# Optimization experiments

Measured on AMD Instinct MI355X. Metric: run time of the kernel, lower is better.

The kernel has to match this reference:

```python
import jax, jax.numpy as jnp
import numpy as np

CAPACITY = 0.5  # top_k = int(seq_len * capacity)

def setup_inputs() -> dict:
    key = jax.random.key(0)
    k1, k2, k3, k4 = jax.random.split(key, 4)
    b, s, d, d_ff = 4, 4096, 1024, 4096
    x = jax.random.normal(k1, (b, s, d), dtype=jnp.float32)
    mask = jnp.ones((b, s), dtype=jnp.bool_)
    # learned params: router (Linear(d,1,bias=False)) and the block MLP
    Wr = jax.random.normal(k2, (d, 1), dtype=jnp.float32) * (d ** -0.5)
    W1 = jax.random.normal(k3, (d, d_ff), dtype=jnp.float32) * (d ** -0.5)
    W2 = jax.random.normal(k4, (d_ff, d), dtype=jnp.float32) * (d_ff ** -0.5)
    return {"x": x, "mask": mask, "Wr": Wr, "W1": W1, "W2": W2}

def reference(x, mask, Wr, W1, W2):
    b, s, d = x.shape
    top_k = int(s * CAPACITY)
    # router logits [b, s]
    logits = (x @ Wr)[..., 0]
    # top-k over sequence dim (torch sorted=False; softmax/gather are
    # permutation-equivariant so sorted top_k gives identical results)
    vals, idx = jax.lax.top_k(logits, top_k)          # [b, k]
    order = jnp.argsort(idx, axis=1)                  # sort selected indices ascending
    sel = jnp.take_along_axis(idx, order, axis=1)     # [b, k] token positions, ascending
    w = jax.nn.softmax(vals, axis=1)                  # softmax over selected logits
    r_w = jnp.take_along_axis(w, order, axis=1)       # weights reordered to match sel
    # gather selected tokens
    fx = jnp.take_along_axis(x, sel[..., None], axis=1)  # [b, k, d]
    # block: residual MLP whose update is scaled by router weights (mask unused by MLP)
    h = jax.nn.silu(fx @ W1) @ W2
    out = fx + h * r_w[..., None]
    # scatter processed tokens back into x
    batch = jnp.arange(b)[:, None]
    hidden_states = x.at[batch, sel].set(out)
    # aux loss: faithful to the original (flat view + flat index set, then BCE-with-logits mean)
    flat_logits = logits.reshape(-1)                  # [b*s]
    targets = jnp.zeros_like(flat_logits).at[sel.reshape(-1)].set(1.0)
    aux_loss = jnp.mean(
        jnp.maximum(flat_logits, 0.0)
        - flat_logits * targets
        + jnp.log1p(jnp.exp(-jnp.abs(flat_logits)))
    )
    return hidden_states, aux_loss
```

## Files before the change

kernel.cpp:

```cpp
#include <hip/hip_runtime.h>
#include <hip/hip_bf16.h>
#include <cstdint>

#define B_ 4
#define S_ 4096
#define D_ 1024
#define DFF_ 4096
#define KSEL_ 2048
#define M_ (B_ * KSEL_)
#define NTOK_ (B_ * S_)

typedef short bf16x8 __attribute__((ext_vector_type(8)));
typedef float f32x4 __attribute__((ext_vector_type(4)));

__device__ inline unsigned short f2bf(float f) {
    union { float f; unsigned int u; } c; c.f = f;
    unsigned int u = c.u;
    unsigned int r = u + 0x7fffu + ((u >> 16) & 1u);
    return (unsigned short)(r >> 16);
}

__global__ __launch_bounds__(256)
void transpose2_bf16(const float* __restrict__ W1, unsigned short* __restrict__ W1bT,
                     const float* __restrict__ W2, unsigned short* __restrict__ W2bT) {
    __shared__ float tile[32][33];
    int id = blockIdx.x;
    const float* src; unsigned short* dst; int R, C, bx, by;
    if (id < (DFF_ / 32) * (D_ / 32)) {
        src = W1; dst = W1bT; R = D_; C = DFF_;
        bx = id % (DFF_ / 32); by = id / (DFF_ / 32);
    } else {
        id -= (DFF_ / 32) * (D_ / 32);
        src = W2; dst = W2bT; R = DFF_; C = D_;
        bx = id % (D_ / 32); by = id / (D_ / 32);
    }
    int c0 = bx * 32, r0 = by * 32;
    for (int i = threadIdx.y; i < 32; i += 8)
        tile[i][threadIdx.x] = src[(size_t)(r0 + i) * C + c0 + threadIdx.x];
    __syncthreads();
    for (int i = threadIdx.y; i < 32; i += 8)
        dst[(size_t)(c0 + i) * R + r0 + threadIdx.x] = f2bf(tile[threadIdx.x][i]);
}

__global__ __launch_bounds__(256)
void router_kernel(const float* __restrict__ x, const float* __restrict__ Wr,
                   float* __restrict__ logits, unsigned short* __restrict__ xb,
                   float* __restrict__ out) {
    int wid = threadIdx.x >> 6, lane = threadIdx.x & 63;
    int row = blockIdx.x * 4 + wid;
    const float* xr = x + (size_t)row * D_;
    unsigned short* xbr = xb + (size_t)row * D_;
    float* outr = out + (size_t)row * D_;
    float acc = 0.f;
#pragma unroll
    for (int j = 0; j < 4; j++) {
        int off = j * 256 + lane * 4;
        float4 v = *(const float4*)(xr + off);
        float4 w = *(const float4*)(Wr + off);
        acc += v.x * w.x + v.y * w.y + v.z * w.z + v.w * w.w;
        *(float4*)(outr + off) = v;
        ushort4 o;
        o.x = f2bf(v.x); o.y = f2bf(v.y); o.z = f2bf(v.z); o.w = f2bf(v.w);
        *(ushort4*)(xbr + off) = o;
    }
#pragma unroll
    for (int s = 32; s; s >>= 1) acc += __shfl_xor(acc, s);
    if (lane == 0) logits[row] = acc;
}

__global__ __launch_bounds__(256)
void rank_partial_kernel(const float* __restrict__ logits, int* __restrict__ rank) {
    __shared__ float lj[512];
    int b  = blockIdx.x >> 7;
    int ic = (blockIdx.x >> 3) & 15;
    int jc = blockIdx.x & 7;
    const float* L = logits + b * S_;
    for (int t = threadIdx.x; t < 512; t += 256) lj[t] = L[jc * 512 + t];
    __syncthreads();
    int i = ic * 256 + threadIdx.x;
    float li = L[i];
    int jbase = jc * 512;
    int r = 0;
    const float4* __restrict__ lj4 = (const float4*)lj;
#pragma unroll 4
    for (int q = 0; q < 128; q++) {
        float4 v = lj4[q];
        int jb = jbase + q * 4;
        r += (v.x > li) | ((v.x == li) & (jb     < i));
        r += (v.y > li) | ((v.y == li) & (jb + 1 < i));
        r += (v.z > li) | ((v.z == li) & (jb + 2 < i));
        r += (v.w > li) | ((v.w == li) & (jb + 3 < i));
    }
    atomicAdd(&rank[b * S_ + i], r);
}

__global__ __launch_bounds__(256)
void compact_kernel(const float* __restrict__ logits, const int* __restrict__ rank,
                    int* __restrict__ flags,
                    int* __restrict__ rowidx, float* __restrict__ rw) {
    __shared__ float lg[S_];
    __shared__ int f[S_];
    __shared__ int tsum[256];
    __shared__ float red[256];
    int b = blockIdx.x;
    const float* L = logits + b * S_;
    const int* R = rank + b * S_;
    int* F = flags + b * S_;
    for (int j = threadIdx.x; j < S_ / 4; j += 256) {
        ((float4*)lg)[j] = ((const float4*)L)[j];
        int4 rk = ((const int4*)R)[j];
        int4 fl;
        fl.x = rk.x < KSEL_; fl.y = rk.y < KSEL_;
        fl.z = rk.z < KSEL_; fl.w = rk.w < KSEL_;
        ((int4*)f)[j] = fl;
        ((int4*)F)[j] = fl;
    }
    __syncthreads();
    float mx = -INFINITY;
    for (int j = threadIdx.x; j < S_; j += 256) mx = fmaxf(mx, lg[j]);
    red[threadIdx.x] = mx; __syncthreads();
    for (int s = 128; s; s >>= 1) {
        if (threadIdx.x < s) red[threadIdx.x] = fmaxf(red[threadIdx.x], red[threadIdx.x + s]);
        __syncthreads();
    }
    float m = red[0];
    __syncthreads();

    float esum = 0.f;
    int s0 = 0;
#pragma unroll
    for (int j = 0; j < 16; j++) {
        int i = threadIdx.x * 16 + j;
        s0 += f[i];
        if (f[i]) esum += expf(lg[i] - m);
    }
    red[threadIdx.x] = esum; __syncthreads();
    for (int s = 128; s; s >>= 1) {
        if (threadIdx.x < s) red[threadIdx.x] += red[threadIdx.x + s];
        __syncthreads();
    }
    float inv = 1.f / red[0];

    tsum[threadIdx.x] = s0; __syncthreads();
    for (int s = 1; s < 256; s <<= 1) {
        int u = (threadIdx.x >= s) ? tsum[threadIdx.x - s] : 0;
        __syncthreads();
        tsum[threadIdx.x] += u;
        __syncthreads();
    }
    int pos = tsum[threadIdx.x] - s0;
    for (int j = 0; j < 16; j++) {
        int i = threadIdx.x * 16 + j;
        if (f[i]) {
            rowidx[b * KSEL_ + pos] = b * S_ + i;
            rw[b * KSEL_ + pos] = expf(lg[i] - m) * inv;
            pos++;
        }
    }
}

__global__ __launch_bounds__(1024)
void loss_fused(const float* __restrict__ logits, const int* __restrict__ flags,
                float* __restrict__ out) {
    __shared__ float red[1024];
    float acc = 0.f;
    for (int i = threadIdx.x; i < NTOK_; i += 1024) {
        float l = logits[i];
        float t = 0.f;
        if (i < S_)
            t = (flags[i] | flags[S_ + i] | flags[2 * S_ + i] | flags[3 * S_ + i]) ? 1.f : 0.f;
        acc += fmaxf(l, 0.f) - l * t + log1pf(expf(-fabsf(l)));
    }
    red[threadIdx.x] = acc; __syncthreads();
    for (int s = 512; s; s >>= 1) {
        if (threadIdx.x < s) red[threadIdx.x] += red[threadIdx.x + s];
        __syncthreads();
    }
    if (threadIdx.x == 0) out[0] = red[0] / (float)NTOK_;
}

template <int N, int K, int SUBS>
__global__ __launch_bounds__(512, 2)
void gemm1_256_kernel(const unsigned short* __restrict__ A,
                      const unsigned short* __restrict__ BT,
                      const int* __restrict__ rowidx,
                      unsigned short* __restrict__ Hout) {
    static_assert(SUBS == 2, "address selection hardcoded for SUBS=2");
    constexpr int BKS = 32;
    constexpr int NSUB = K / BKS;
    constexpr int NSTEPS = SUBS * NSUB;
    constexpr int NT = N / 256;
    constexpr int MG = M_ / (256 * SUBS);
    constexpr int NWG = NT * MG;
    constexpr int CPX = NWG / 8;
    __shared__ __attribute__((aligned(16))) unsigned short As[4][256 * BKS];
    __shared__ __attribute__((aligned(16))) unsigned short Bs[4][256 * BKS];

    const int tid = threadIdx.x;
    const int w = tid >> 6, lane = tid & 63;
    const int wm = w >> 2, wn = w & 3;

    int wgid = blockIdx.y * NT + blockIdx.x;
    int swz = (wgid & 7) * CPX + (wgid >> 3);
    const int tile_n = (swz % NT) * 256;
    const int mgrp   = swz / NT;

    const int srow = tid >> 2;
    const int lchunk = (tid & 3) ^ ((tid >> 3) & 3);
    const uint64_t abase = (uint64_t)(uintptr_t)A;
    const uint64_t bbase = (uint64_t)(uintptr_t)BT;
    uint64_t aaddr[SUBS][2], baddr[2];
#pragma unroll
    for (int s = 0; s < SUBS; ++s)
#pragma unroll
        for (int i = 0; i < 2; ++i) {
            int r = i * 128 + srow;
            int ar = rowidx[(mgrp * SUBS + s) * 256 + r];
            aaddr[s][i] = abase + ((uint64_t)ar * K + (uint64_t)lchunk * 8) * 2ull;
        }
#pragma unroll
    for (int i = 0; i < 2; ++i) {
        int r = i * 128 + srow;
        baddr[i] = bbase + ((uint64_t)(tile_n + r) * K + (uint64_t)lchunk * 8) * 2ull;
    }

    auto gload = [&](unsigned short* lds, uint64_t gaddr) {
        __builtin_amdgcn_global_load_lds(
            (const __attribute__((address_space(1))) unsigned int*)(uintptr_t)gaddr,
            (__attribute__((address_space(3))) unsigned int*)lds, 16, 0, 0);
    };
    auto stageA = [&](int g, int slot) {
        const uint64_t koff = (uint64_t)(g & (NSUB - 1)) * (BKS * 2);
        const uint64_t a0 = (g >= NSUB) ? aaddr[1][0] : aaddr[0][0];
        const uint64_t a1 = (g >= NSUB) ? aaddr[1][1] : aaddr[0][1];
        gload(&As[slot][(0 * 512 + w * 64) * 8], a0 + koff);
        gload(&As[slot][(1 * 512 + w * 64) * 8], a1 + koff);
    };
    auto stageB = [&](int g, int slot) {
        const uint64_t koff = (uint64_t)(g & (NSUB - 1)) * (BKS * 2);
        gload(&Bs[slot][(0 * 512 + w * 64) * 8], baddr[0] + koff);
        gload(&Bs[slot][(1 * 512 + w * 64) * 8], baddr[1] + koff);
    };

    f32x4 acc[8][4];
#pragma unroll
    for (int i = 0; i < 8; i++)
#pragma unroll
        for (int j = 0; j < 4; j++) acc[i][j] = (f32x4){0.f, 0.f, 0.f, 0.f};

    const int lr = lane & 15, quad = lane >> 4;
    const int xo = (quad ^ ((lr >> 1) & 3)) * 16;

    auto flush = [&](int s) {
        const int tm = (mgrp * SUBS + s) * 256 + wm * 128;
#pragma unroll
        for (int m4 = 0; m4 < 8; ++m4)
#pragma unroll
            for (int r = 0; r < 4; ++r) {
                int m = tm + m4 * 16 + quad * 4 + r;
#pragma unroll
                for (int n4 = 0; n4 < 4; ++n4) {
                    int col = tile_n + wn * 64 + n4 * 16 + lr;
                    float v = acc[m4][n4][r];
                    v = v / (1.f + __expf(-v));
                    Hout[(uint64_t)m * N + col] = f2bf(v);
                }
            }
    };

    stageA(0, 0); stageB(0, 0);
    stageA(1, 1); stageB(1, 1);
    stageA(2, 2); stageB(2, 2);
    asm volatile("s_waitcnt vmcnt(8)" ::: "memory");
    asm volatile("s_barrier" ::: "memory");

#pragma unroll 1
    for (int t = 0; t < NSTEPS; ++t) {
        const int c = t & 3, pslot = (t + 3) & 3;
        const bool dost = (t + 3 < NSTEPS);
        const char* Ab = (const char*)&As[c][0];
        const char* Bb = (const char*)&Bs[c][0];

        bf16x8 bfr[4];
        {
            bf16x8 af[4];
#pragma unroll
            for (int m4 = 0; m4 < 4; ++m4)
                af[m4] = *(const bf16x8*)(Ab + (wm * 128 + m4 * 16 + lr) * 64 + xo);
#pragma unroll
            for (int n4 = 0; n4 < 4; ++n4)
                bfr[n4] = *(const bf16x8*)(Bb + (wn * 64 + n4 * 16 + lr) * 64 + xo);
            if (dost) stageA(t + 3, pslot);
            asm volatile("s_barrier" ::: "memory");
            asm volatile("s_waitcnt lgkmcnt(0)" ::: "memory");
            __builtin_amdgcn_sched_barrier(0);
            __builtin_amdgcn_s_setprio(1);
#pragma unroll
            for (int m4 = 0; m4 < 4; ++m4)
#pragma unroll
                for (int n4 = 0; n4 < 4; ++n4)
                    acc[m4][n4] = __builtin_amdgcn_mfma_f32_16x16x32_bf16(
                        af[m4], bfr[n4], acc[m4][n4], 0, 0, 0);
            __builtin_amdgcn_s_setprio(0);
            asm volatile("s_barrier" ::: "memory");
        }

        {
            bf16x8 af[4];
#pragma unroll
            for (int m4 = 0; m4 < 4; ++m4)
                af[m4] = *(const bf16x8*)(Ab + (wm * 128 + 64 + m4 * 16 + lr) * 64 + xo);
            if (dost) stageB(t + 3, pslot);
            asm volatile("s_barrier" ::: "memory");
            asm volatile("s_waitcnt lgkmcnt(0)" ::: "memory");
            __builtin_amdgcn_sched_barrier(0);
            __builtin_amdgcn_s_setprio(1);
#pragma unroll
            for (int m4 = 0; m4 < 4; ++m4)
#pragma unroll
                for (int n4 = 0; n4 < 4; ++n4)
                    acc[4 + m4][n4] = __builtin_amdgcn_mfma_f32_16x16x32_bf16(
                        af[m4], bfr[n4], acc[4 + m4][n4], 0, 0, 0);
            __builtin_amdgcn_s_setprio(0);
            if (t + 3 < NSTEPS) {
                asm volatile("s_waitcnt vmcnt(8)" ::: "memory");
            } else if (t + 2 < NSTEPS) {
                asm volatile("s_waitcnt vmcnt(4)" ::: "memory");
            } else if (t + 1 < NSTEPS) {
                asm volatile("s_waitcnt vmcnt(0)" ::: "memory");
            }
            asm volatile("s_barrier" ::: "memory");
        }

        if ((t & (NSUB - 1)) == (NSUB - 1) && (t + 1) < NSTEPS) {
            flush(t / NSUB);
#pragma unroll
            for (int i = 0; i < 8; i++)
#pragma unroll
                for (int j = 0; j < 4; j++) acc[i][j] = (f32x4){0.f, 0.f, 0.f, 0.f};
        }
    }
    flush(SUBS - 1);
}

template <int MODE, int N, int K, int SUBS>
__global__ __launch_bounds__(512, 2)
void gemm_pipe_kernel(const unsigned short* __restrict__ A,
                      const unsigned short* __restrict__ BT,
                      const int* __restrict__ rowidx,
                      const float* __restrict__ rw,
                      const float* __restrict__ x,
                      unsigned short* __restrict__ Hout,
                      float* __restrict__ Out) {
    constexpr int BM = 128, BN = 256, BK = 64;
    constexpr int KI = K / BK;
    constexpr int NT = N / BN;
    constexpr int MG = M_ / (BM * SUBS);
    constexpr int NWG = NT * MG;
    constexpr int CPX = NWG / 8;
    __shared__ __attribute__((aligned(16))) unsigned short As[3][BM * BK];
    __shared__ __attribute__((aligned(16))) unsigned short Bs[3][BN * BK];

    const int tid = threadIdx.x;
    const int w = tid >> 6, lane = tid & 63;
    const int wm = w >> 2, wn = w & 3;

    int wgid = blockIdx.y * NT + blockIdx.x;
    int swz = (wgid & 7) * CPX + (wgid >> 3);
    const int tile_n = (swz % NT) * BN;
    const int mgrp   = (swz / NT);

    const int srow = lane >> 3;
    const int sw = (lane & 7) ^ srow;
    const uint64_t abase = (uint64_t)(uintptr_t)A;
    const uint64_t bbase = (uint64_t)(uintptr_t)BT;
    uint64_t aaddr[SUBS][2], baddr[4];
#pragma unroll
    for (int s = 0; s < SUBS; ++s)
#pragma unroll
        for (int t = 0; t < 2; ++t) {
            int r = t * 64 + w * 8 + srow;
            int am = (mgrp * SUBS + s) * BM + r;
            int ar = (MODE == 1) ? rowidx[am] : am;
            aaddr[s][t] = abase + ((uint64_t)ar * K + (uint64_t)sw * 8) * 2ull;
        }
#pragma unroll
    for (int t = 0; t < 4; ++t) {
        int r = t * 64 + w * 8 + srow;
        baddr[t] = bbase + ((uint64_t)(tile_n + r) * K + (uint64_t)sw * 8) * 2ull;
    }

    auto gload = [&](unsigned short* lds, uint64_t gaddr) {
        __builtin_amdgcn_global_load_lds(
            (const __attribute__((address_space(1))) unsigned int*)(uintptr_t)gaddr,
            (__attribute__((address_space(3))) unsigned int*)lds, 16, 0, 0);
    };

    f32x4 acc[4][4];
#pragma unroll
    for (int i = 0; i < 4; i++)
#pragma unroll
        for (int j = 0; j < 4; j++) acc[i][j] = (f32x4){0.f, 0.f, 0.f, 0.f};

#pragma unroll
    for (int p = 0; p < 2; ++p) {
        const uint64_t koff = (uint64_t)p * (BK * 2);
        gload(&As[p][(0 * 64 + w * 8) * BK], aaddr[0][0] + koff);
        gload(&As[p][(1 * 64 + w * 8) * BK], aaddr[0][1] + koff);
#pragma unroll
        for (int t = 0; t < 4; ++t)
            gload(&Bs[p][(t * 64 + w * 8) * BK], baddr[t] + koff);
    }
    asm volatile("s_waitcnt vmcnt(6)" ::: "memory");
    asm volatile("s_barrier" ::: "memory");

    const int lr = lane & 15, quad = lane >> 4;
    int c = 0;
#pragma unroll
    for (int s = 0; s < SUBS; ++s) {
#pragma unroll 1
        for (int kt = 0; kt < KI; ++kt) {
            int pre = c + 2; if (pre >= 3) pre -= 3;
            const char* Abase_l = (const char*)&As[c][0];
            const char* Bbase_l = (const char*)&Bs[c][0];
            const bool cross = (kt + 2 >= KI);
            const bool do_stage = (s < SUBS - 1) || (kt + 2 < KI);
            const uint64_t sa0 = cross ? aaddr[(s + 1 < SUBS) ? s + 1 : s][0]
                                       : aaddr[s][0];
            const uint64_t sa1 = cross ? aaddr[(s + 1 < SUBS) ? s + 1 : s][1]
                                       : aaddr[s][1];
            const uint64_t koff = (uint64_t)((kt + 2) & (KI - 1)) * (BK * 2);

            {
                bf16x8 af[4], bfr[4];
                const int xo = (quad ^ (lr & 7)) * 16;
#pragma unroll
                for (int m4 = 0; m4 < 4; ++m4) {
                    int row = wm * 64 + m4 * 16 + lr;
                    af[m4] = *(const bf16x8*)(Abase_l + row * (BK * 2) + xo);
                }
#pragma unroll
                for (int n4 = 0; n4 < 4; ++n4) {
                    int col = wn * 64 + n4 * 16 + lr;
                    bfr[n4] = *(const bf16x8*)(Bbase_l + col * (BK * 2) + xo);
                }
                if (do_stage) {
                    gload(&As[pre][(0 * 64 + w * 8) * BK], sa0 + koff);
                    gload(&As[pre][(1 * 64 + w * 8) * BK], sa1 + koff);
                    gload(&Bs[pre][(w * 8) * BK], baddr[0] + koff);
                }
                asm volatile("s_barrier" ::: "memory");
                asm volatile("s_waitcnt lgkmcnt(0)" ::: "memory");
                __builtin_amdgcn_sched_barrier(0);
                __builtin_amdgcn_s_setprio(1);
#pragma unroll
                for (int m4 = 0; m4 < 4; ++m4)
#pragma unroll
                    for (int n4 = 0; n4 < 4; ++n4)
                        acc[m4][n4] = __builtin_amdgcn_mfma_f32_16x16x32_bf16(
                            af[m4], bfr[n4], acc[m4][n4], 0, 0, 0);
                __builtin_amdgcn_s_setprio(0);
                asm volatile("s_barrier" ::: "memory");
            }

            {
                bf16x8 af[4], bfr[4];
                const int xo = ((4 + quad) ^ (lr & 7)) * 16;
#pragma unroll
                for (int m4 = 0; m4 < 4; ++m4) {
                    int row = wm * 64 + m4 * 16 + lr;
                    af[m4] = *(const bf16x8*)(Abase_l + row * (BK * 2) + xo);
                }
#pragma unroll
                for (int n4 = 0; n4 < 4; ++n4) {
                    int col = wn * 64 + n4 * 16 + lr;
                    bfr[n4] = *(const bf16x8*)(Bbase_l + col * (BK * 2) + xo);
                }
                if (do_stage) {
#pragma unroll
                    for (int t = 1; t < 4; ++t)
                        gload(&Bs[pre][(t * 64 + w * 8) * BK], baddr[t] + koff);
                }
                asm volatile("s_barrier" ::: "memory");
                asm volatile("s_waitcnt lgkmcnt(0)" ::: "memory");
                __builtin_amdgcn_sched_barrier(0);
                __builtin_amdgcn_s_setprio(1);
#pragma unroll
                for (int m4 = 0; m4 < 4; ++m4)
#pragma unroll
                    for (int n4 = 0; n4 < 4; ++n4)
                        acc[m4][n4] = __builtin_amdgcn_mfma_f32_16x16x32_bf16(
                            af[m4], bfr[n4], acc[m4][n4], 0, 0, 0);
                __builtin_amdgcn_s_setprio(0);
                if (do_stage) {
                    asm volatile("s_waitcnt vmcnt(6)" ::: "memory");
                } else if (kt + 2 == KI) {
                    asm volatile("s_waitcnt vmcnt(0)" ::: "memory");
                }
                asm volatile("s_barrier" ::: "memory");
                c += 1; if (c >= 3) c = 0;
            }
        }

        if (MODE == 1) {
            const int tile_m = (mgrp * SUBS + s) * BM;
#pragma unroll
            for (int m4 = 0; m4 < 4; ++m4)
#pragma unroll
                for (int r = 0; r < 4; ++r) {
                    int m = tile_m + wm * 64 + m4 * 16 + quad * 4 + r;
#pragma unroll
                    for (int n4 = 0; n4 < 4; ++n4) {
                        int col = tile_n + wn * 64 + n4 * 16 + lr;
                        float v = acc[m4][n4][r];
                        v = v / (1.f + __expf(-v));
                        Hout[(uint64_t)m * N + col] = f2bf(v);
                    }
                }
            if (s + 1 < SUBS) {
#pragma unroll
                for (int i = 0; i < 4; i++)
#pragma unroll
                    for (int j = 0; j < 4; j++)
                        acc[i][j] = (f32x4){0.f, 0.f, 0.f, 0.f};
            }
        }
    }

    if (MODE == 2) {
        const int tile_m = mgrp * SUBS * BM;
#pragma unroll
        for (int m4 = 0; m4 < 4; ++m4)
#pragma unroll
            for (int r = 0; r < 4; ++r) {
                int m = tile_m + wm * 64 + m4 * 16 + quad * 4 + r;
                int grow = rowidx[m];
                float wgt = rw[m];
                uint64_t rb = (uint64_t)grow * D_;
#pragma unroll
                for (int n4 = 0; n4 < 4; ++n4) {
                    int col = tile_n + wn * 64 + n4 * 16 + lr;
                    Out[rb + col] = x[rb + col] + acc[m4][n4][r] * wgt;
                }
            }
    }
}

extern "C" void kernel_launch(void* const* d_in, const int* in_sizes, int n_in,
                              void* d_out, int out_size, void* d_ws, size_t ws_size,
                              hipStream_t stream) {
    const float* x  = (const float*)d_in[0];
    const float* Wr = (const float*)d_in[2];
    const float* W1 = (const float*)d_in[3];
    const float* W2 = (const float*)d_in[4];
    float* out = (float*)d_out;

    char* ws = (char*)d_ws;
    size_t off = 0;
    auto alloc = [&](size_t bytes) {
        char* p = ws + off;
        off = (off + bytes + 255) & ~(size_t)255;
        return p;
    };
    unsigned short* xb   = (unsigned short*)alloc((size_t)NTOK_ * D_ * 2);
    unsigned short* W1bT = (unsigned short*)alloc((size_t)DFF_ * D_ * 2);
    unsigned short* W2bT = (unsigned short*)alloc((size_t)D_ * DFF_ * 2);
    unsigned short* H    = (unsigned short*)alloc((size_t)M_ * DFF_ * 2);
    float* logits  = (float*)alloc(NTOK_ * 4);
    int*   rank    = (int*)alloc(NTOK_ * 4);
    int*   flags   = (int*)alloc(NTOK_ * 4);
    int*   rowidx  = (int*)alloc(M_ * 4);
    float* rwp     = (float*)alloc(M_ * 4);

    (void)hipMemsetAsync(rank, 0, NTOK_ * 4, stream);

    transpose2_bf16<<<2 * (DFF_ / 32) * (D_ / 32), dim3(32, 8), 0, stream>>>(
        W1, W1bT, W2, W2bT);
    router_kernel<<<NTOK_ / 4, 256, 0, stream>>>(x, Wr, logits, xb, out);
    rank_partial_kernel<<<512, 256, 0, stream>>>(logits, rank);
    compact_kernel<<<B_, 256, 0, stream>>>(logits, rank, flags, rowidx, rwp);
    loss_fused<<<1, 1024, 0, stream>>>(logits, flags, out + (size_t)NTOK_ * D_);
    gemm1_256_kernel<DFF_, D_, 2><<<dim3(DFF_ / 256, M_ / 512), 512, 0, stream>>>(
        xb, W1bT, rowidx, H);
    gemm_pipe_kernel<2, D_, DFF_, 1><<<dim3(D_ / 256, M_ / 128), 512, 0, stream>>>(
        H, W2bT, rowidx, rwp, x, nullptr, out);
}
```

Baseline: 363.4 us.

## Restructure GEMM1 into BK=64 double-buffered half-tile pipeline and parallelize aux loss

The first MLP GEMM now uses 64-wide K tiles with two LDS buffers split into halves. Loads for the next tiles are staged in quarter pieces interleaved with four MFMA sub-blocks per tile, and the LDS layout uses an 8-chunk XOR swizzle. This aims to cut barrier and waitcnt overhead per unit of MFMA work and to spread global-to-LDS traffic more evenly, at the cost of a shallower prefetch depth and more complex scheduling. Separately, the single-block aux-loss reduction is replaced by a 64-block partial-sum kernel plus a small final wavefront reduction, adding one extra launch.

New measurement: 390.8 us. 1.08x slower.

```diff
diff --git a/kernel.cpp b/kernel.cpp
--- a/kernel.cpp
+++ b/kernel.cpp
@@ -159,42 +159,47 @@
     }
 }
 
-__global__ __launch_bounds__(1024)
-void loss_fused(const float* __restrict__ logits, const int* __restrict__ flags,
-                float* __restrict__ out) {
-    __shared__ float red[1024];
-    float acc = 0.f;
-    for (int i = threadIdx.x; i < NTOK_; i += 1024) {
-        float l = logits[i];
-        float t = 0.f;
-        if (i < S_)
-            t = (flags[i] | flags[S_ + i] | flags[2 * S_ + i] | flags[3 * S_ + i]) ? 1.f : 0.f;
-        acc += fmaxf(l, 0.f) - l * t + log1pf(expf(-fabsf(l)));
-    }
-    red[threadIdx.x] = acc; __syncthreads();
-    for (int s = 512; s; s >>= 1) {
+__global__ __launch_bounds__(256)
+void loss_kernel(const float* __restrict__ logits, const int* __restrict__ flags,
+                 float* __restrict__ partials) {
+    __shared__ float red[256];
+    int i = blockIdx.x * 256 + threadIdx.x;
+    float l = logits[i];
+    float t = 0.f;
+    if (i < S_)
+        t = (flags[i] | flags[S_ + i] | flags[2 * S_ + i] | flags[3 * S_ + i]) ? 1.f : 0.f;
+    float v = fmaxf(l, 0.f) - l * t + log1pf(expf(-fabsf(l)));
+    red[threadIdx.x] = v; __syncthreads();
+    for (int s = 128; s; s >>= 1) {
         if (threadIdx.x < s) red[threadIdx.x] += red[threadIdx.x + s];
         __syncthreads();
     }
-    if (threadIdx.x == 0) out[0] = red[0] / (float)NTOK_;
+    if (threadIdx.x == 0) partials[blockIdx.x] = red[0];
+}
+
+__global__ void loss_final(const float* __restrict__ partials, float* __restrict__ out) {
+    float v = partials[threadIdx.x];
+#pragma unroll
+    for (int s = 32; s; s >>= 1) v += __shfl_xor(v, s);
+    if (threadIdx.x == 0) out[0] = v / (float)NTOK_;
 }
 
 template <int N, int K, int SUBS>
 __global__ __launch_bounds__(512, 2)
-void gemm1_256_kernel(const unsigned short* __restrict__ A,
-                      const unsigned short* __restrict__ BT,
-                      const int* __restrict__ rowidx,
-                      unsigned short* __restrict__ Hout) {
+void gemm1_8p_kernel(const unsigned short* __restrict__ A,
+                     const unsigned short* __restrict__ BT,
+                     const int* __restrict__ rowidx,
+                     unsigned short* __restrict__ Hout) {
     static_assert(SUBS == 2, "address selection hardcoded for SUBS=2");
-    constexpr int BKS = 32;
-    constexpr int NSUB = K / BKS;
-    constexpr int NSTEPS = SUBS * NSUB;
+    constexpr int BK = 64;
+    constexpr int KT = K / BK;
+    constexpr int TT = SUBS * KT;
     constexpr int NT = N / 256;
     constexpr int MG = M_ / (256 * SUBS);
     constexpr int NWG = NT * MG;
     constexpr int CPX = NWG / 8;
-    __shared__ __attribute__((aligned(16))) unsigned short As[4][256 * BKS];
-    __shared__ __attribute__((aligned(16))) unsigned short Bs[4][256 * BKS];
+    __shared__ __attribute__((aligned(16))) unsigned short As[2][2][128 * BK];
+    __shared__ __attribute__((aligned(16))) unsigned short Bs[2][2][128 * BK];
 
     const int tid = threadIdx.x;
     const int w = tid >> 6, lane = tid & 63;
@@ -205,23 +210,19 @@
     const int tile_n = (swz % NT) * 256;
     const int mgrp   = swz / NT;
 
-    const int srow = tid >> 2;
-    const int lchunk = (tid & 3) ^ ((tid >> 3) & 3);
+    const int srow = lane >> 3;
+    const int sw = (lane & 7) ^ srow;
     const uint64_t abase = (uint64_t)(uintptr_t)A;
     const uint64_t bbase = (uint64_t)(uintptr_t)BT;
-    uint64_t aaddr[SUBS][2], baddr[2];
-#pragma unroll
-    for (int s = 0; s < SUBS; ++s)
-#pragma unroll
-        for (int i = 0; i < 2; ++i) {
-            int r = i * 128 + srow;
-            int ar = rowidx[(mgrp * SUBS + s) * 256 + r];
-            aaddr[s][i] = abase + ((uint64_t)ar * K + (uint64_t)lchunk * 8) * 2ull;
-        }
-#pragma unroll
-    for (int i = 0; i < 2; ++i) {
-        int r = i * 128 + srow;
-        baddr[i] = bbase + ((uint64_t)(tile_n + r) * K + (uint64_t)lchunk * 8) * 2ull;
+    uint64_t aaddr0[4], aaddr1[4], baddr[4];
+#pragma unroll
+    for (int h = 0; h < 4; ++h) {
+        int r0 = (mgrp * SUBS + 0) * 256 + h * 64 + w * 8 + srow;
+        int r1 = (mgrp * SUBS + 1) * 256 + h * 64 + w * 8 + srow;
+        aaddr0[h] = abase + ((uint64_t)rowidx[r0] * K + (uint64_t)sw * 8) * 2ull;
+        aaddr1[h] = abase + ((uint64_t)rowidx[r1] * K + (uint64_t)sw * 8) * 2ull;
+        int rb = tile_n + h * 64 + w * 8 + srow;
+        baddr[h] = bbase + ((uint64_t)rb * K + (uint64_t)sw * 8) * 2ull;
     }
 
     auto gload = [&](unsigned short* lds, uint64_t gaddr) {
@@ -229,17 +230,21 @@
             (const __attribute__((address_space(1))) unsigned int*)(uintptr_t)gaddr,
             (__attribute__((address_space(3))) unsigned int*)lds, 16, 0, 0);
     };
-    auto stageA = [&](int g, int slot) {
-        const uint64_t koff = (uint64_t)(g & (NSUB - 1)) * (BKS * 2);
-        const uint64_t a0 = (g >= NSUB) ? aaddr[1][0] : aaddr[0][0];
-        const uint64_t a1 = (g >= NSUB) ? aaddr[1][1] : aaddr[0][1];
-        gload(&As[slot][(0 * 512 + w * 64) * 8], a0 + koff);
-        gload(&As[slot][(1 * 512 + w * 64) * 8], a1 + koff);
+    auto stageAh = [&](int tt, int half) {
+        const uint64_t koff = (uint64_t)(tt & (KT - 1)) * (BK * 2);
+        const int slot = tt & 1;
+#pragma unroll
+        for (int g = 0; g < 2; ++g) {
+            const uint64_t a = (tt >= KT) ? aaddr1[half * 2 + g] : aaddr0[half * 2 + g];
+            gload(&As[slot][half][(g * 64 + w * 8) * BK], a + koff);
+        }
     };
-    auto stageB = [&](int g, int slot) {
-        const uint64_t koff = (uint64_t)(g & (NSUB - 1)) * (BKS * 2);
-        gload(&Bs[slot][(0 * 512 + w * 64) * 8], baddr[0] + koff);
-        gload(&Bs[slot][(1 * 512 + w * 64) * 8], baddr[1] + koff);
+    auto stageBh = [&](int tt, int half) {
+        const uint64_t koff = (uint64_t)(tt & (KT - 1)) * (BK * 2);
+        const int slot = tt & 1;
+#pragma unroll
+        for (int g = 0; g < 2; ++g)
+            gload(&Bs[slot][half][(g * 64 + w * 8) * BK], baddr[half * 2 + g] + koff);
     };
 
     f32x4 acc[8][4];
@@ -249,7 +254,6 @@
         for (int j = 0; j < 4; j++) acc[i][j] = (f32x4){0.f, 0.f, 0.f, 0.f};
 
     const int lr = lane & 15, quad = lane >> 4;
-    const int xo = (quad ^ ((lr >> 1) & 3)) * 16;
 
     auto flush = [&](int s) {
         const int tm = (mgrp * SUBS + s) * 256 + wm * 128;
@@ -268,72 +272,79 @@
             }
     };
 
-    stageA(0, 0); stageB(0, 0);
-    stageA(1, 1); stageB(1, 1);
-    stageA(2, 2); stageB(2, 2);
-    asm volatile("s_waitcnt vmcnt(8)" ::: "memory");
+    stageAh(0, 0); stageAh(0, 1); stageBh(0, 0); stageBh(0, 1);
+    stageBh(1, 0); stageBh(1, 1);
+    asm volatile("s_waitcnt vmcnt(4)" ::: "memory");
     asm volatile("s_barrier" ::: "memory");
 
 #pragma unroll 1
-    for (int t = 0; t < NSTEPS; ++t) {
-        const int c = t & 3, pslot = (t + 3) & 3;
-        const bool dost = (t + 3 < NSTEPS);
-        const char* Ab = (const char*)&As[c][0];
-        const char* Bb = (const char*)&Bs[c][0];
-
-        bf16x8 bfr[4];
-        {
-            bf16x8 af[4];
-#pragma unroll
-            for (int m4 = 0; m4 < 4; ++m4)
-                af[m4] = *(const bf16x8*)(Ab + (wm * 128 + m4 * 16 + lr) * 64 + xo);
-#pragma unroll
-            for (int n4 = 0; n4 < 4; ++n4)
-                bfr[n4] = *(const bf16x8*)(Bb + (wn * 64 + n4 * 16 + lr) * 64 + xo);
-            if (dost) stageA(t + 3, pslot);
-            asm volatile("s_barrier" ::: "memory");
-            asm volatile("s_waitcnt lgkmcnt(0)" ::: "memory");
-            __builtin_amdgcn_sched_barrier(0);
-            __builtin_amdgcn_s_setprio(1);
-#pragma unroll
-            for (int m4 = 0; m4 < 4; ++m4)
-#pragma unroll
-                for (int n4 = 0; n4 < 4; ++n4)
-                    acc[m4][n4] = __builtin_amdgcn_mfma_f32_16x16x32_bf16(
-                        af[m4], bfr[n4], acc[m4][n4], 0, 0, 0);
-            __builtin_amdgcn_s_setprio(0);
-            asm volatile("s_barrier" ::: "memory");
+    for (int it = 0; it < TT / 2; ++it) {
+        const int t = 2 * it;
+#pragma unroll
+        for (int tp = 0; tp < 2; ++tp) {
+            const int slot = tp;
+            bf16x8 bfr[4][2];
+#pragma unroll
+            for (int mb = 0; mb < 4; ++mb) {
+                bf16x8 af[2][2];
+#pragma unroll
+                for (int d = 0; d < 2; ++d)
+#pragma unroll
+                    for (int kk = 0; kk < 2; ++kk) {
+                        int lrow = (2 * mb + d) * 16 + lr;
+                        int xo = (((kk * 4 + quad) ^ (lr & 7)) * 16);
+                        af[d][kk] = *(const bf16x8*)((const char*)&As[slot][wm][0]
+                                        + lrow * (BK * 2) + xo);
+                    }
+                if (mb == 0) {
+#pragma unroll
+                    for (int n4 = 0; n4 < 4; ++n4)
+#pragma unroll
+                        for (int kk = 0; kk < 2; ++kk) {
+                            int lrow = (wn & 1) * 64 + n4 * 16 + lr;
+                            int xo = (((kk * 4 + quad) ^ (lr & 7)) * 16);
+                            bfr[n4][kk] = *(const bf16x8*)((const char*)&Bs[slot][wn >> 1][0]
+                                            + lrow * (BK * 2) + xo);
+                        }
+                }
+                if (tp == 0) {
+                    if (mb == 0)      stageAh(t + 1, 0);
+                    else if (mb == 1) stageAh(t + 1, 1);
+                    else if (mb == 2) { if (t + 2 < TT) stageBh(t + 2, 0); }
+                    else              { if (t + 2 < TT) stageBh(t + 2, 1); }
+                } else {
+                    if (mb == 0)      { if (t + 2 < TT) stageAh(t + 2, 0); }
+                    else if (mb == 1) { if (t + 2 < TT) stageAh(t + 2, 1); }
+                    else if (mb == 2) { if (t + 3 < TT) stageBh(t + 3, 0); }
+                    else              { if (t + 3 < TT) stageBh(t + 3, 1); }
+                }
+                asm volatile("s_barrier" ::: "memory");
+                asm volatile("s_waitcnt lgkmcnt(0)" ::: "memory");
+                __builtin_amdgcn_sched_barrier(0);
+                __builtin_amdgcn_s_setprio(1);
+#pragma unroll
+                for (int kk = 0; kk < 2; ++kk)
+#pragma unroll
+                    for (int d = 0; d < 2; ++d)
+#pragma unroll
+                        for (int n4 = 0; n4 < 4; ++n4)
+                            acc[2 * mb + d][n4] = __builtin_amdgcn_mfma_f32_16x16x32_bf16(
+                                af[d][kk], bfr[n4][kk], acc[2 * mb + d][n4], 0, 0, 0);
+                __builtin_amdgcn_s_setprio(0);
+                if (mb == 3) {
+                    if (tp == 0) {
+                        if (t + 2 < TT) { asm volatile("s_waitcnt vmcnt(4)" ::: "memory"); }
+                        else            { asm volatile("s_waitcnt vmcnt(0)" ::: "memory"); }
+                    } else {
+                        if (t + 3 < TT) { asm volatile("s_waitcnt vmcnt(4)" ::: "memory"); }
+                        else            { asm volatile("s_waitcnt vmcnt(0)" ::: "memory"); }
+                    }
+                }
+                asm volatile("s_barrier" ::: "memory");
+            }
         }
-
-        {
-            bf16x8 af[4];
-#pragma unroll
-            for (int m4 = 0; m4 < 4; ++m4)
-                af[m4] = *(const bf16x8*)(Ab + (wm * 128 + 64 + m4 * 16 + lr) * 64 + xo);
-            if (dost) stageB(t + 3, pslot);
-            asm volatile("s_barrier" ::: "memory");
-            asm volatile("s_waitcnt lgkmcnt(0)" ::: "memory");
-            __builtin_amdgcn_sched_barrier(0);
-            __builtin_amdgcn_s_setprio(1);
-#pragma unroll
-            for (int m4 = 0; m4 < 4; ++m4)
-#pragma unroll
-                for (int n4 = 0; n4 < 4; ++n4)
-                    acc[4 + m4][n4] = __builtin_amdgcn_mfma_f32_16x16x32_bf16(
-                        af[m4], bfr[n4], acc[4 + m4][n4], 0, 0, 0);
-            __builtin_amdgcn_s_setprio(0);
-            if (t + 3 < NSTEPS) {
-                asm volatile("s_waitcnt vmcnt(8)" ::: "memory");
-            } else if (t + 2 < NSTEPS) {
-                asm volatile("s_waitcnt vmcnt(4)" ::: "memory");
-            } else if (t + 1 < NSTEPS) {
-                asm volatile("s_waitcnt vmcnt(0)" ::: "memory");
-            }
-            asm volatile("s_barrier" ::: "memory");
-        }
-
-        if ((t & (NSUB - 1)) == (NSUB - 1) && (t + 1) < NSTEPS) {
-            flush(t / NSUB);
+        if (t + 2 == KT) {
+            flush(0);
 #pragma unroll
             for (int i = 0; i < 8; i++)
 #pragma unroll
@@ -571,6 +582,7 @@
     int*   flags   = (int*)alloc(NTOK_ * 4);
     int*   rowidx  = (int*)alloc(M_ * 4);
     float* rwp     = (float*)alloc(M_ * 4);
+    float* partials = (float*)alloc(64 * 4);
 
     (void)hipMemsetAsync(rank, 0, NTOK_ * 4, stream);
 
@@ -579,8 +591,9 @@
     router_kernel<<<NTOK_ / 4, 256, 0, stream>>>(x, Wr, logits, xb, out);
     rank_partial_kernel<<<512, 256, 0, stream>>>(logits, rank);
     compact_kernel<<<B_, 256, 0, stream>>>(logits, rank, flags, rowidx, rwp);
-    loss_fused<<<1, 1024, 0, stream>>>(logits, flags, out + (size_t)NTOK_ * D_);
-    gemm1_256_kernel<DFF_, D_, 2><<<dim3(DFF_ / 256, M_ / 512), 512, 0, stream>>>(
+    loss_kernel<<<NTOK_ / 256, 256, 0, stream>>>(logits, flags, partials);
+    loss_final<<<1, 64, 0, stream>>>(partials, out + (size_t)NTOK_ * D_);
+    gemm1_8p_kernel<DFF_, D_, 2><<<dim3(DFF_ / 256, M_ / 512), 512, 0, stream>>>(
         xb, W1bT, rowidx, H);
     gemm_pipe_kernel<2, D_, DFF_, 1><<<dim3(D_ / 256, M_ / 128), 512, 0, stream>>>(
         H, W2bT, rowidx, rwp, x, nullptr, out);
```
